# Performance work log

Hardware: AMD Instinct MI355X
Metric: run time of the kernel (lower is better)

The kernel has to match this reference:

```python
import jax, jax.numpy as jnp
import numpy as np
import math

B, S, H = 4, 4096, 64
WINDOW = 2


def setup_inputs() -> dict:
    key = jax.random.key(0)
    ks = jax.random.split(key, 7)
    s = 0.05
    return {
        "feature": jax.random.normal(ks[0], (B, S, H), dtype=jnp.float32),
        "Wq": jax.random.normal(ks[1], (H, H), dtype=jnp.float32) * s,
        "bq": jax.random.normal(ks[2], (H,), dtype=jnp.float32) * s,
        "Wk": jax.random.normal(ks[3], (H, H), dtype=jnp.float32) * s,
        "bk": jax.random.normal(ks[4], (H,), dtype=jnp.float32) * s,
        "Wv": jax.random.normal(ks[5], (H, H), dtype=jnp.float32) * s,
        "bv": jax.random.normal(ks[6], (H,), dtype=jnp.float32) * s,
    }


def reference(feature, Wq, bq, Wk, bk, Wv, bv):
    b, seq, d_k = feature.shape
    # torch nn.Linear: y = x @ W.T + b
    q = feature @ Wq.T + bq  # [B,S,H]
    k = feature @ Wk.T + bk
    v = feature @ Wv.T + bv

    # banded 0/1 mask, |i-j| <= window, then softmax over the FULL row
    # (faithful to the original: zeros outside the band also get exp(0)=1 weight)
    idx = jnp.arange(seq)
    band = (jnp.abs(idx[:, None] - idx[None, :]) <= WINDOW).astype(jnp.float32)  # [S,S]
    weights = jax.nn.softmax(band, axis=-1)  # [S,S]

    # locally-averaged K: weights @ k, shared across batch
    mixed_k = jnp.einsum('st,bth->bsh', weights, k)  # [B,S,H]
    scores = jnp.einsum('bsh,bth->bst', q, mixed_k) / math.sqrt(d_k)  # [B,S,S]
    attn = jax.nn.softmax(scores, axis=-1)
    out = jnp.einsum('bst,bth->bsh', attn, v)  # [B,S,H]
    return out
```

## Files before the change

### kernel.cpp

```cpp
#include <hip/hip_runtime.h>
#include <hip/hip_bf16.h>
#include <math.h>

#define SEQ 4096
#define HD  64
#define NBATCH 4

#define EM1   1.71828182845904523536f
#define INVD5 (1.0f/(4096.f + 5.f*EM1))
#define INVD4 (1.0f/(4096.f + 4.f*EM1))
#define INVD3 (1.0f/(4096.f + 3.f*EM1))

typedef __attribute__((ext_vector_type(8))) short short8;
typedef __attribute__((ext_vector_type(4))) float f32x4;

__device__ __forceinline__ f32x4 mfma16(short8 a, short8 b, f32x4 c) {
    return __builtin_amdgcn_mfma_f32_16x16x32_bf16(a, b, c, 0, 0, 0);
}

__device__ __forceinline__ short bfs(float x) {
    __hip_bfloat16 h = __float2bfloat16(x);
    return *(short*)&h;
}

__device__ __forceinline__ short8 pack8(float4 a, float4 b) {
    short8 r;
    r[0] = bfs(a.x); r[1] = bfs(a.y); r[2] = bfs(a.z); r[3] = bfs(a.w);
    r[4] = bfs(b.x); r[5] = bfs(b.y); r[6] = bfs(b.z); r[7] = bfs(b.w);
    return r;
}

__device__ __forceinline__ float b2f(__hip_bfloat16 h) { return __bfloat162float(h); }
__device__ __forceinline__ float sb2f(short s) {
    return __uint_as_float(((unsigned)(unsigned short)s) << 16);
}

__global__ __launch_bounds__(256) void wpack_kernel(
    const float* __restrict__ Wq, const float* __restrict__ Wk,
    const float* __restrict__ Wv, __hip_bfloat16* __restrict__ Wb)
{
    const int blk = blockIdx.x, tid = threadIdx.x;
    const float* W = (blk == 0) ? Wq : (blk == 1) ? Wk : Wv;
    const float s = (blk == 0) ? 0.125f : 1.f;
    const float* src = W + tid * 16;
    float4 a0 = *(const float4*)(src);
    float4 a1 = *(const float4*)(src + 4);
    float4 a2 = *(const float4*)(src + 8);
    float4 a3 = *(const float4*)(src + 12);
    a0.x*=s; a0.y*=s; a0.z*=s; a0.w*=s;
    a1.x*=s; a1.y*=s; a1.z*=s; a1.w*=s;
    a2.x*=s; a2.y*=s; a2.z*=s; a2.w*=s;
    a3.x*=s; a3.y*=s; a3.z*=s; a3.w*=s;
    __hip_bfloat16* dst = Wb + blk * 4096 + tid * 16;
    *(short8*)(dst)     = pack8(a0, a1);
    *(short8*)(dst + 8) = pack8(a2, a3);
}

__global__ __launch_bounds__(256) void projm_kernel(
    const float* __restrict__ feat, const __hip_bfloat16* __restrict__ Wb,
    const float* __restrict__ bq, const float* __restrict__ bk,
    const float* __restrict__ bv,
    __hip_bfloat16* __restrict__ qsb, float* __restrict__ kpart,
    float* __restrict__ vpart, __hip_bfloat16* __restrict__ Mpart,
    float* __restrict__ kedge)
{
    __shared__ __hip_bfloat16 kT[64 * 40];
    __shared__ __hip_bfloat16 vT[64 * 40];
    __shared__ __hip_bfloat16 lvt[64 * 40];
    __shared__ float kred[4][32];
    __shared__ float vred[4][32];

    const int tid  = threadIdx.x;
    const int wave = tid >> 6, lane = tid & 63;
    const int rg = wave >> 1, cg = wave & 1;
    const int quad = lane >> 4, ln = lane & 15;
    const int R0 = blockIdx.x * 32;
    const int b  = R0 >> 12;
    const int t0 = R0 & (SEQ - 1);
    const int chunk = blockIdx.x & 127;

    short8 af0, af1;
    {
        const float* fp = feat + (size_t)(R0 + rg * 16 + ln) * HD + quad * 8;
        af0 = pack8(*(const float4*)(fp),      *(const float4*)(fp + 4));
        af1 = pack8(*(const float4*)(fp + 32), *(const float4*)(fp + 36));
    }

    short8 hf0, hf1;
    const bool hflag = (rg == 0) ? (t0 > 0) : (t0 < SEQ - 32);
    {
        const int hrow = (rg == 0) ? (t0 - 2 + ln) : (t0 + 32 + ln);
        if (ln < 2 && hflag) {
            const float* fp = feat + ((size_t)(b << 12) + hrow) * HD + quad * 8;
            hf0 = pack8(*(const float4*)(fp),      *(const float4*)(fp + 4));
            hf1 = pack8(*(const float4*)(fp + 32), *(const float4*)(fp + 36));
        } else {
            #pragma unroll
            for (int j = 0; j < 8; ++j) { hf0[j] = 0; hf1[j] = 0; }
        }
    }

    const float* Bs[3] = {bq, bk, bv};

    #pragma unroll
    for (int m = 0; m < 3; ++m) {
        const __hip_bfloat16* W = Wb + m * 4096;
        const float* bias = Bs[m];
        #pragma unroll
        for (int ctp = 0; ctp < 2; ++ctp) {
            const int col = cg * 32 + ctp * 16 + ln;
            const __hip_bfloat16* wp = W + col * 64 + quad * 8;
            short8 b0 = *(const short8*)(wp);
            short8 b1 = *(const short8*)(wp + 32);
            f32x4 c = {};
            c = mfma16(af0, b0, c);
            c = mfma16(af1, b1, c);

            if (m == 0) {
                const float bl = bias[col] * 0.125f;
                #pragma unroll
                for (int r = 0; r < 4; ++r)
                    qsb[(size_t)(R0 + rg * 16 + quad * 4 + r) * HD + col] =
                        __float2bfloat16(c[r] + bl);
            } else if (m == 1) {
                const float bl = bias[col];
                float tot = c[0] + c[1] + c[2] + c[3];
                tot += __shfl_xor(tot, 16);
                tot += __shfl_xor(tot, 32);
                if (quad == 0) kred[wave][ctp * 16 + ln] = tot;
                #pragma unroll
                for (int r = 0; r < 4; ++r)
                    kT[col * 40 + rg * 16 + quad * 4 + r] =
                        __float2bfloat16(c[r] + bl);
            } else {
                const float bl = bias[col];
                float tot = c[0] + c[1] + c[2] + c[3];
                tot += __shfl_xor(tot, 16);
                tot += __shfl_xor(tot, 32);
                if (quad == 0) vred[wave][ctp * 16 + ln] = tot;
                #pragma unroll
                for (int r = 0; r < 4; ++r)
                    vT[col * 40 + 2 + rg * 16 + quad * 4 + r] =
                        __float2bfloat16(c[r] + bl);
                f32x4 hc = {};
                hc = mfma16(hf0, b0, hc);
                hc = mfma16(hf1, b1, hc);
                if (quad == 0) {
                    const int base = (rg == 0) ? 0 : 34;
                    vT[col * 40 + base]     = __float2bfloat16(hflag ? hc[0] + bl : 0.f);
                    vT[col * 40 + base + 1] = __float2bfloat16(hflag ? hc[1] + bl : 0.f);
                }
            }
        }
    }
    __syncthreads();

    if (tid < 64) {
        const int col = tid, cg2 = col >> 5, cl = col & 31;
        kpart[(size_t)blockIdx.x * 64 + col] =
            kred[cg2][cl] + kred[2 + cg2][cl] + 32.f * bk[col];
        vpart[(size_t)blockIdx.x * 64 + col] =
            vred[cg2][cl] + vred[2 + cg2][cl] + 32.f * bv[col];
    }

    {
        const int h = tid & 63;
        const int tb = wave * 8;
        short8 v0 = *(const short8*)&vT[h * 40 + tb];
        short8 v1 = *(const short8*)&vT[h * 40 + tb + 8];
        float w[12];
        #pragma unroll
        for (int j = 0; j < 8; ++j) w[j] = sb2f(v0[j]);
        #pragma unroll
        for (int j = 0; j < 4; ++j) w[8 + j] = sb2f(v1[j]);
        short8 o;
        #pragma unroll
        for (int i = 0; i < 8; ++i)
            o[i] = bfs(w[i] + w[i+1] + w[i+2] + w[i+3] + w[i+4]);
        *(short8*)&lvt[h * 40 + tb] = o;
    }

    if (chunk == 0) {
        const int t = tid >> 6, h = tid & 63;
        kedge[b * 512 + t * 64 + h] = b2f(kT[h * 40 + t]);
    } else if (chunk == 127) {
        const int t = tid >> 6, h = tid & 63;
        kedge[b * 512 + (4 + t) * 64 + h] = b2f(kT[h * 40 + 28 + t]);
    }
    __syncthreads();

    __hip_bfloat16* mp = Mpart + (size_t)(b * 128 + chunk) * 4096;
    {
        const int strip = wave;
        short8 a = *(const short8*)&kT[(strip * 16 + ln) * 40 + quad * 8];
        #pragma unroll
        for (int ct = 0; ct < 4; ++ct) {
            short8 bb = *(const short8*)&lvt[(ct * 16 + ln) * 40 + quad * 8];
            f32x4 acc = {};
            acc = mfma16(a, bb, acc);
            #pragma unroll
            for (int r = 0; r < 4; ++r)
                mp[(strip * 16 + quad * 4 + r) * 64 + ct * 16 + ln] =
                    __float2bfloat16(acc[r]);
        }
    }
}

__global__ __launch_bounds__(256) void redprep_kernel(
    const __hip_bfloat16* __restrict__ Mpart, const float* __restrict__ kpart,
    const float* __restrict__ vpart, const float* __restrict__ kedge,
    __hip_bfloat16* __restrict__ MTm, float* __restrict__ mktotF,
    float* __restrict__ ktotF, float* __restrict__ VDs,
    float* __restrict__ VtotF)
{
    __shared__ float redv[256 * 8];
    __shared__ float red[4][64];
    __shared__ float red2[4][64];
    const int b = blockIdx.y, x = blockIdx.x;
    const int tid = threadIdx.x;

    if (x < 64) {
        const int h1 = x;
        const int ci = tid >> 3;
        const int vp = tid & 7;
        float a[8] = {};
        #pragma unroll
        for (int j = 0; j < 4; ++j) {
            const int c = ci * 4 + j;
            short8 v = *(const short8*)&Mpart[(size_t)(b * 128 + c) * 4096
                                              + h1 * 64 + vp * 8];
            #pragma unroll
            for (int e = 0; e < 8; ++e) a[e] += sb2f(v[e]);
        }
        #pragma unroll
        for (int e = 0; e < 8; ++e) redv[tid * 8 + e] = a[e];
        __syncthreads();
        if (tid < 64) {
            const int h2 = tid;
            float s = 0.f;
            for (int ci2 = 0; ci2 < 32; ++ci2)
                s += redv[ci2 * 64 + h2];
            MTm[(size_t)b * 4096 + h2 * 64 + h1] =
                __float2bfloat16((EM1 * INVD5) * s);
        }
        return;
    }

    const int g = tid >> 6, h2 = tid & 63;
    {
        float kp = 0.f, vp = 0.f;
        for (int j = 0; j < 32; ++j) {
            kp += kpart[(size_t)(b * 128 + g * 32 + j) * 64 + h2];
            vp += vpart[(size_t)(b * 128 + g * 32 + j) * 64 + h2];
        }
        red[g][h2] = kp;
        red2[g][h2] = vp;
    }
    __syncthreads();
    if (tid < 64) {
        const int hh = tid;
        const float kt = red[0][hh] + red[1][hh] + red[2][hh] + red[3][hh];
        const float vt = red2[0][hh] + red2[1][hh] + red2[2][hh] + red2[3][hh];
        const float e0 = kedge[b * 512 + 0 * 64 + hh];
        const float e1 = kedge[b * 512 + 1 * 64 + hh];
        const float e2 = kedge[b * 512 + 2 * 64 + hh];
        const float e3 = kedge[b * 512 + 3 * 64 + hh];
        const float f0 = kedge[b * 512 + 4 * 64 + hh];
        const float f1 = kedge[b * 512 + 5 * 64 + hh];
        const float f2 = kedge[b * 512 + 6 * 64 + hh];
        const float f3 = kedge[b * 512 + 7 * 64 + hh];
        const float Sint = 5.f*kt - 4.f*e0 - 3.f*e1 - 2.f*e2 - e3
                         - f0 - 2.f*f1 - 3.f*f2 - 4.f*f3;
        const float SlocD = Sint * INVD5
                          + (e0+e1+e2 + f1+f2+f3) * INVD3
                          + (e0+e1+e2+e3 + f0+f1+f2+f3) * INVD4;
        mktotF[b * 64 + hh] = kt * (4092.f*INVD5 + 2.f*INVD4 + 2.f*INVD3) + EM1 * SlocD;
        ktotF[b * 64 + hh]  = kt;
        VDs[b * 64 + hh]    = INVD5 * vt;
        VtotF[b * 64 + hh]  = vt;
    }
}

__global__ __launch_bounds__(64) void out_kernel(
    const __hip_bfloat16* __restrict__ qsb, const __hip_bfloat16* __restrict__ MTm,
    const float* __restrict__ mktotF, const float* __restrict__ ktotF,
    const float* __restrict__ VDs, const float* __restrict__ VtotF,
    float* __restrict__ out)
{
    const int tid = threadIdx.x;
    const int quad = tid >> 4, ln = tid & 15;
    const int R0 = blockIdx.x * 16;
    const int b = R0 >> 12;

    short8 qa0, qa1;
    {
        const __hip_bfloat16* qp = qsb + (size_t)(R0 + ln) * HD + quad * 8;
        qa0 = *(const short8*)qp;
        qa1 = *(const short8*)(qp + 32);
    }

    const __hip_bfloat16* mtb = MTm + (size_t)b * 4096;
    f32x4 acc[4];
    #pragma unroll
    for (int ct = 0; ct < 4; ++ct) {
        short8 b0 = *(const short8*)(mtb + (ct * 16 + ln) * 64 + quad * 8);
        short8 b1 = *(const short8*)(mtb + (ct * 16 + ln) * 64 + 32 + quad * 8);
        f32x4 c = {};
        c = mfma16(qa0, b0, c);
        c = mfma16(qa1, b1, c);
        acc[ct] = c;
    }

    short8 mk0, mk1, kt0, kt1;
    #pragma unroll
    for (int j = 0; j < 8; ++j) {
        mk0[j] = bfs(mktotF[b * 64 + quad * 8 + j]);
        mk1[j] = bfs(mktotF[b * 64 + 32 + quad * 8 + j]);
        kt0[j] = bfs(ktotF[b * 64 + quad * 8 + j]);
        kt1[j] = bfs(ktotF[b * 64 + 32 + quad * 8 + j]);
    }
    f32x4 accd = {}, acck = {};
    accd = mfma16(qa0, mk0, accd);
    accd = mfma16(qa1, mk1, accd);
    acck = mfma16(qa0, kt0, acck);
    acck = mfma16(qa1, kt1, acck);

    float vt[4], vd[4];
    #pragma unroll
    for (int ct = 0; ct < 4; ++ct) {
        vt[ct] = VtotF[b * 64 + ct * 16 + ln];
        vd[ct] = VDs[b * 64 + ct * 16 + ln];
    }

    float inv[4];
    #pragma unroll
    for (int r = 0; r < 4; ++r) inv[r] = 1.f / (4096.f + accd[r]);

    #pragma unroll
    for (int ct = 0; ct < 4; ++ct)
        #pragma unroll
        for (int r = 0; r < 4; ++r)
            out[(size_t)(R0 + quad * 4 + r) * HD + ct * 16 + ln] =
                (vt[ct] + acc[ct][r] + acck[r] * vd[ct]) * inv[r];
}

extern "C" void kernel_launch(void* const* d_in, const int* in_sizes, int n_in,
                              void* d_out, int out_size, void* d_ws, size_t ws_size,
                              hipStream_t stream)
{
    const float* feat = (const float*)d_in[0];
    const float* Wq = (const float*)d_in[1];
    const float* bq = (const float*)d_in[2];
    const float* Wk = (const float*)d_in[3];
    const float* bk = (const float*)d_in[4];
    const float* Wv = (const float*)d_in[5];
    const float* bv = (const float*)d_in[6];
    float* out = (float*)d_out;

    char* ws = (char*)d_ws;
    __hip_bfloat16* qsb    = (__hip_bfloat16*)(ws + 0);
    __hip_bfloat16* Mpart  = (__hip_bfloat16*)(ws + (2u << 20));
    float*          kpart  = (float*)(ws + (6u << 20));
    float*          vpart  = (float*)(ws + (6u << 20) + 131072);
    float*          kedge  = (float*)(ws + (6u << 20) + 262144);
    __hip_bfloat16* MTm    = (__hip_bfloat16*)(ws + (6u << 20) + 270336);
    float*          mktotF = (float*)(ws + (6u << 20) + 303104);
    float*          ktotF  = (float*)(ws + (6u << 20) + 304128);
    float*          VDs    = (float*)(ws + (6u << 20) + 305152);
    float*          VtotF  = (float*)(ws + (6u << 20) + 306176);
    __hip_bfloat16* Wb     = (__hip_bfloat16*)(ws + (6u << 20) + 307200);

    wpack_kernel<<<dim3(3), dim3(256), 0, stream>>>(Wq, Wk, Wv, Wb);
    projm_kernel<<<dim3(512), dim3(256), 0, stream>>>(
        feat, Wb, bq, bk, bv, qsb, kpart, vpart, Mpart, kedge);
    redprep_kernel<<<dim3(65, NBATCH), dim3(256), 0, stream>>>(
        Mpart, kpart, vpart, kedge, MTm, mktotF, ktotF, VDs, VtotF);
    out_kernel<<<dim3(1024), dim3(64), 0, stream>>>(
        qsb, MTm, mktotF, ktotF, VDs, VtotF, out);
}
```

Measured before the change: 83.42 us.

## Fuse reduction kernel into projection via last-block-per-batch atomic counter

Removes the separate redprep kernel launch by having projm blocks increment a per-batch atomic counter. The last block to finish for each batch then reduces Mpart, kpart and vpart and writes MTm and the totals. The counter is reset in wpack. This saves one launch and its gap, but the cross-chunk reduction now runs on only 4 blocks (one per batch) instead of 260, so it is much less parallel and may become a serial tail.

```diff
diff --git a/kernel.cpp b/kernel.cpp
--- a/kernel.cpp
+++ b/kernel.cpp
@@ -37,9 +37,11 @@
 
 __global__ __launch_bounds__(256) void wpack_kernel(
     const float* __restrict__ Wq, const float* __restrict__ Wk,
-    const float* __restrict__ Wv, __hip_bfloat16* __restrict__ Wb)
+    const float* __restrict__ Wv, __hip_bfloat16* __restrict__ Wb,
+    int* __restrict__ Mcount)
 {
     const int blk = blockIdx.x, tid = threadIdx.x;
+    if (blk == 0 && tid < NBATCH) Mcount[tid] = 0;
     const float* W = (blk == 0) ? Wq : (blk == 1) ? Wk : Wv;
     const float s = (blk == 0) ? 0.125f : 1.f;
     const float* src = W + tid * 16;
@@ -62,13 +64,20 @@
     const float* __restrict__ bv,
     __hip_bfloat16* __restrict__ qsb, float* __restrict__ kpart,
     float* __restrict__ vpart, __hip_bfloat16* __restrict__ Mpart,
-    float* __restrict__ kedge)
+    float* __restrict__ kedge, int* __restrict__ Mcount,
+    __hip_bfloat16* __restrict__ MTm, float* __restrict__ mktotF,
+    float* __restrict__ ktotF, float* __restrict__ VDs,
+    float* __restrict__ VtotF)
 {
     __shared__ __hip_bfloat16 kT[64 * 40];
     __shared__ __hip_bfloat16 vT[64 * 40];
     __shared__ __hip_bfloat16 lvt[64 * 40];
     __shared__ float kred[4][32];
     __shared__ float vred[4][32];
+    __shared__ __hip_bfloat16 stage[4][16][64];
+    __shared__ float redk[4][64];
+    __shared__ float redv2[4][64];
+    __shared__ int amLast;
 
     const int tid  = threadIdx.x;
     const int wave = tid >> 6, lane = tid & 63;
@@ -204,63 +213,70 @@
                     __float2bfloat16(acc[r]);
         }
     }
-}
-
-__global__ __launch_bounds__(256) void redprep_kernel(
-    const __hip_bfloat16* __restrict__ Mpart, const float* __restrict__ kpart,
-    const float* __restrict__ vpart, const float* __restrict__ kedge,
-    __hip_bfloat16* __restrict__ MTm, float* __restrict__ mktotF,
-    float* __restrict__ ktotF, float* __restrict__ VDs,
-    float* __restrict__ VtotF)
-{
-    __shared__ float redv[256 * 8];
-    __shared__ float red[4][64];
-    __shared__ float red2[4][64];
-    const int b = blockIdx.y, x = blockIdx.x;
-    const int tid = threadIdx.x;
-
-    if (x < 64) {
-        const int h1 = x;
-        const int ci = tid >> 3;
-        const int vp = tid & 7;
-        float a[8] = {};
-        #pragma unroll
-        for (int j = 0; j < 4; ++j) {
-            const int c = ci * 4 + j;
-            short8 v = *(const short8*)&Mpart[(size_t)(b * 128 + c) * 4096
-                                              + h1 * 64 + vp * 8];
+
+    __syncthreads();
+    if (tid == 0) {
+        __threadfence();
+        amLast = (atomicAdd(&Mcount[b], 1) == 127);
+    }
+    __syncthreads();
+    if (!amLast) return;
+    __threadfence();
+
+    {
+        const int ln8 = lane >> 3, vp = lane & 7;
+        for (int r = 0; r < 16; ++r) {
+            const int h1 = wave * 16 + r;
+            float a[8] = {};
+            for (int it = 0; it < 16; ++it) {
+                const int c = it * 8 + ln8;
+                short8 v = *(const short8*)&Mpart[(size_t)(b * 128 + c) * 4096
+                                                  + h1 * 64 + vp * 8];
+                #pragma unroll
+                for (int e = 0; e < 8; ++e) a[e] += sb2f(v[e]);
+            }
             #pragma unroll
-            for (int e = 0; e < 8; ++e) a[e] += sb2f(v[e]);
-        }
-        #pragma unroll
-        for (int e = 0; e < 8; ++e) redv[tid * 8 + e] = a[e];
-        __syncthreads();
-        if (tid < 64) {
-            const int h2 = tid;
-            float s = 0.f;
-            for (int ci2 = 0; ci2 < 32; ++ci2)
-                s += redv[ci2 * 64 + h2];
-            MTm[(size_t)b * 4096 + h2 * 64 + h1] =
-                __float2bfloat16((EM1 * INVD5) * s);
-        }
-        return;
-    }
-
-    const int g = tid >> 6, h2 = tid & 63;
-    {
-        float kp = 0.f, vp = 0.f;
+            for (int e = 0; e < 8; ++e) {
+                a[e] += __shfl_xor(a[e], 8);
+                a[e] += __shfl_xor(a[e], 16);
+                a[e] += __shfl_xor(a[e], 32);
+            }
+            if (ln8 == 0) {
+                #pragma unroll
+                for (int e = 0; e < 8; ++e)
+                    stage[wave][r][vp * 8 + e] =
+                        __float2bfloat16((EM1 * INVD5) * a[e]);
+            }
+        }
+    }
+    {
+        const int g = tid >> 6, hh = tid & 63;
+        float kp = 0.f, vp2 = 0.f;
         for (int j = 0; j < 32; ++j) {
-            kp += kpart[(size_t)(b * 128 + g * 32 + j) * 64 + h2];
-            vp += vpart[(size_t)(b * 128 + g * 32 + j) * 64 + h2];
-        }
-        red[g][h2] = kp;
-        red2[g][h2] = vp;
-    }
-    __syncthreads();
+            kp  += kpart[(size_t)(b * 128 + g * 32 + j) * 64 + hh];
+            vp2 += vpart[(size_t)(b * 128 + g * 32 + j) * 64 + hh];
+        }
+        redk[g][hh] = kp;
+        redv2[g][hh] = vp2;
+    }
+    __syncthreads();
+
+    #pragma unroll
+    for (int i = 0; i < 2; ++i) {
+        const int tsk = i * 256 + tid;
+        const int h2 = tsk & 63, oct = tsk >> 6;
+        const int w2 = oct >> 1, rb = (oct & 1) * 8;
+        short8 o;
+        #pragma unroll
+        for (int j = 0; j < 8; ++j)
+            o[j] = *(short*)&stage[w2][rb + j][h2];
+        *(short8*)&MTm[(size_t)b * 4096 + h2 * 64 + oct * 8] = o;
+    }
+
     if (tid < 64) {
         const int hh = tid;
-        const float kt = red[0][hh] + red[1][hh] + red[2][hh] + red[3][hh];
-        const float vt = red2[0][hh] + red2[1][hh] + red2[2][hh] + red2[3][hh];
+        const float kt = redk[0][hh] + redk[1][hh] + redk[2][hh] + redk[3][hh];
+        const float vt = redv2[0][hh] + redv2[1][hh] + redv2[2][hh] + redv2[3][hh];
         const float e0 = kedge[b * 512 + 0 * 64 + hh];
         const float e1 = kedge[b * 512 + 1 * 64 + hh];
         const float e2 = kedge[b * 512 + 2 * 64 + hh];
@@ -369,12 +385,12 @@
     float*          VDs    = (float*)(ws + (6u << 20) + 305152);
     float*          VtotF  = (float*)(ws + (6u << 20) + 306176);
     __hip_bfloat16* Wb     = (__hip_bfloat16*)(ws + (6u << 20) + 307200);
-
-    wpack_kernel<<<dim3(3), dim3(256), 0, stream>>>(Wq, Wk, Wv, Wb);
+    int*            Mcount = (int*)(ws + (6u << 20) + 331776);
+
+    wpack_kernel<<<dim3(3), dim3(256), 0, stream>>>(Wq, Wk, Wv, Wb, Mcount);
     projm_kernel<<<dim3(512), dim3(256), 0, stream>>>(
-        feat, Wb, bq, bk, bv, qsb, kpart, vpart, Mpart, kedge);
-    redprep_kernel<<<dim3(65, NBATCH), dim3(256), 0, stream>>>(
-        Mpart, kpart, vpart, kedge, MTm, mktotF, ktotF, VDs, VtotF);
+        feat, Wb, bq, bk, bv, qsb, kpart, vpart, Mpart, kedge,
+        Mcount, MTm, mktotF, ktotF, VDs, VtotF);
     out_kernel<<<dim3(1024), dim3(64), 0, stream>>>(
         qsb, MTm, mktotF, ktotF, VDs, VtotF, out);
 }
```

After: 127.1 us. +52.3%, slower.
